# Kernel tuning notes

Hardware: AMD Instinct MI355X
Metric: run time of the kernel (lower is better)

## Reference

```python
import jax, jax.numpy as jnp
import numpy as np
from jax import lax

H_PARAM = 10
DMAX = 3
L = 2 * H_PARAM * H_PARAM + 2 * H_PARAM + 1  # 221 chain length
HEIGHT = H_PARAM + 1   # 11
WIDTH = 2 * H_PARAM + 1  # 21
B, N = 256, 128
INIT_STD = 1e-9


def setup_inputs() -> dict:
    key = jax.random.key(0)
    k1, k2 = jax.random.split(key)
    samples = jax.random.normal(k1, (B, N, HEIGHT, WIDTH, DMAX), dtype=jnp.float32)
    tensors1 = INIT_STD * jax.random.normal(k2, (L, DMAX, DMAX, DMAX), dtype=jnp.float32)
    bias_mat = jnp.eye(DMAX, dtype=jnp.float32)[None, :, :]  # [1, D, D]
    return {"samples": samples, "tensors1": tensors1, "bias_mat": bias_mat}


def reference(samples, tensors1, bias_mat):
    b, n = samples.shape[0], samples.shape[1]
    D = tensors1.shape[-1]
    # [B*N, HW, D] then keep only the L positions actually contracted
    s = samples.reshape(b * n, -1, D)[:, : tensors1.shape[0], :]
    s_seq = jnp.moveaxis(s, 1, 0)  # [L, BN, D]
    eye_bias = bias_mat[0]         # [D, D]
    init = jnp.zeros((b * n, D), dtype=samples.dtype).at[:, 0].set(1.0)

    def step(vec, xs):
        x, T = xs  # x: [BN, D], T: [D, D, D]
        mats = jnp.einsum('bd,lrd->blr', x, T) + eye_bias  # [BN, D, D]
        vec = jnp.einsum('bl,blr->br', vec, mats)          # [BN, D]
        return vec, None

    vec, _ = lax.scan(step, init, (s_seq, tensors1))
    return vec.reshape(b, n, D)
```

## Files before the change

kernel.cpp:

```cpp
#include <hip/hip_runtime.h>

#define BN        32768
#define ESTRIDE   693
#define L_REAL    221
#define CHUNK     14
#define PH        7
#define PDW       21
#define SLICE_DW  1344
#define NGRP      4

__device__ __forceinline__ void dma12(const float* g, float* l) {
    __builtin_amdgcn_global_load_lds(
        (const __attribute__((address_space(1))) void*)g,
        (__attribute__((address_space(3))) void*)l,
        12, 0, 0);
}

__global__ __launch_bounds__(256, 8)
void mps_worker(const float* __restrict__ samples,
                const float* __restrict__ tensors,
                float* __restrict__ ws)
{
    __shared__ float lds_x[4 * SLICE_DW];

    const int tid = threadIdx.x;
    const int eg  = blockIdx.x >> 2;
    const int cg  = blockIdx.x & 3;
    const int e0  = eg * 64;
    const int w   = tid >> 6;
    const int b   = tid & 63;
    const int ck  = __builtin_amdgcn_readfirstlane(cg * 4 + w);

    unsigned g7[7];
    #pragma unroll
    for (int k = 0; k < 7; ++k) {
        int i  = k * 64 + b;
        int e  = i / 7;
        int pc = i - e * 7;
        g7[k] = (unsigned)(e0 + e) * ESTRIDE + (unsigned)(ck * (CHUNK * 3) + pc * 3);
    }

    float* slice = lds_x + w * SLICE_DW;
    float P[9] = {1.f, 0.f, 0.f, 0.f, 1.f, 0.f, 0.f, 0.f, 1.f};

    #pragma unroll
    for (int k = 0; k < 7; ++k)
        dma12(samples + g7[k], slice + k * 192);

    #pragma unroll
    for (int p = 0; p < 2; ++p) {
        asm volatile("s_waitcnt vmcnt(0)" ::: "memory");
        __builtin_amdgcn_sched_barrier(0);

        float xq[PDW];
        const float* Xs = slice + b * PDW;
        #pragma unroll
        for (int j = 0; j < PDW; ++j) xq[j] = Xs[j];
        asm volatile("s_waitcnt lgkmcnt(0)" ::: "memory");
        __builtin_amdgcn_sched_barrier(0);

        if (p == 0) {
            #pragma unroll
            for (int k = 0; k < 7; ++k)
                dma12(samples + g7[k] + PDW, slice + k * 192);
        }

        #pragma unroll
        for (int s = 0; s < PH; ++s) {
            const int l = ck * CHUNK + p * PH + s;
            if (l < L_REAL) {
                const float* Tg = tensors + l * 27;
                float Ts[27];
                #pragma unroll
                for (int j = 0; j < 27; ++j) Ts[j] = Tg[j];

                const float x0 = xq[s * 3 + 0];
                const float x1 = xq[s * 3 + 1];
                const float x2 = xq[s * 3 + 2];

                float E[9];
                #pragma unroll
                for (int l2 = 0; l2 < 3; ++l2)
                    #pragma unroll
                    for (int r = 0; r < 3; ++r)
                        E[l2 * 3 + r] = x0 * Ts[l2 * 9 + r * 3 + 0]
                                      + x1 * Ts[l2 * 9 + r * 3 + 1]
                                      + x2 * Ts[l2 * 9 + r * 3 + 2];

                float PN[9];
                #pragma unroll
                for (int i = 0; i < 3; ++i)
                    #pragma unroll
                    for (int r = 0; r < 3; ++r)
                        PN[i * 3 + r] = P[i * 3 + 0] * E[0 + r]
                                      + P[i * 3 + 1] * E[3 + r]
                                      + P[i * 3 + 2] * E[6 + r];
                #pragma unroll
                for (int k = 0; k < 9; ++k) P[k] += PN[k];
            }
        }
    }

    __syncthreads();
    {
        float* pb = lds_x + tid * 9;
        #pragma unroll
        for (int k = 0; k < 9; ++k) pb[k] = P[k];
    }
    __syncthreads();

    if (tid < 64) {
        float G[9];
        #pragma unroll
        for (int k = 0; k < 9; ++k) G[k] = lds_x[tid * 9 + k];
        #pragma unroll
        for (int w2 = 1; w2 < 4; ++w2) {
            const float* q = lds_x + (w2 * 64 + tid) * 9;
            float N[9];
            #pragma unroll
            for (int i = 0; i < 3; ++i)
                #pragma unroll
                for (int r = 0; r < 3; ++r)
                    N[i * 3 + r] = G[i * 3 + 0] * q[0 + r]
                                 + G[i * 3 + 1] * q[3 + r]
                                 + G[i * 3 + 2] * q[6 + r];
            #pragma unroll
            for (int k = 0; k < 9; ++k) G[k] = N[k];
        }
        #pragma unroll
        for (int k = 0; k < 9; ++k)
            ws[((size_t)(cg * 9 + k) << 15) + (size_t)(e0 + tid)] = G[k];
    }
}

__global__ __launch_bounds__(256)
void mps_combine(const float* __restrict__ ws, float* __restrict__ out)
{
    const int e = blockIdx.x * 256 + threadIdx.x;
    float v0 = ws[(size_t)(0 << 15) + e];
    float v1 = ws[(size_t)(1 << 15) + e];
    float v2 = ws[(size_t)(2 << 15) + e];
    #pragma unroll
    for (int g = 1; g < NGRP; ++g) {
        float q[9];
        #pragma unroll
        for (int k = 0; k < 9; ++k)
            q[k] = ws[((size_t)(g * 9 + k) << 15) + e];
        float n0 = v0 * q[0] + v1 * q[3] + v2 * q[6];
        float n1 = v0 * q[1] + v1 * q[4] + v2 * q[7];
        float n2 = v0 * q[2] + v1 * q[5] + v2 * q[8];
        v0 = n0; v1 = n1; v2 = n2;
    }
    float* o = out + (size_t)e * 3;
    o[0] = v0; o[1] = v1; o[2] = v2;
}

extern "C" void kernel_launch(void* const* d_in, const int* in_sizes, int n_in,
                              void* d_out, int out_size, void* d_ws, size_t ws_size,
                              hipStream_t stream)
{
    const float* samples = (const float*)d_in[0];
    const float* tensors = (const float*)d_in[1];
    float* out = (float*)d_out;
    float* ws  = (float*)d_ws;
    (void)ws_size;

    mps_worker<<<dim3(512 * NGRP), dim3(256), 0, stream>>>(samples, tensors, ws);
    mps_combine<<<dim3(BN / 256), dim3(256), 0, stream>>>(ws, out);
}
```

Baseline: 35.21 us.

## Replace LDS DMA staging with direct per-thread global loads of sample chunk

Drops the two-phase global_load_lds staging of sample slices through LDS and instead has each thread load its 42 contiguous floats straight from global memory into registers, then run all 14 chain steps in one loop. This removes the LDS round trip, explicit waitcnt barriers and the mid-kernel double-buffer reissue. It shrinks LDS use and lowers the occupancy hint from 8 to 6 waves to allow more registers. The cost is that per-thread loads with a 693-float stride are poorly coalesced, and register pressure rises.

```diff
diff --git a/kernel.cpp b/kernel.cpp
--- a/kernel.cpp
+++ b/kernel.cpp
@@ -4,24 +4,15 @@
 #define ESTRIDE   693
 #define L_REAL    221
 #define CHUNK     14
-#define PH        7
-#define PDW       21
-#define SLICE_DW  1344
+#define CDW       42
 #define NGRP      4
 
-__device__ __forceinline__ void dma12(const float* g, float* l) {
-    __builtin_amdgcn_global_load_lds(
-        (const __attribute__((address_space(1))) void*)g,
-        (__attribute__((address_space(3))) void*)l,
-        12, 0, 0);
-}
-
-__global__ __launch_bounds__(256, 8)
+__global__ __launch_bounds__(256, 6)
 void mps_worker(const float* __restrict__ samples,
                 const float* __restrict__ tensors,
                 float* __restrict__ ws)
 {
-    __shared__ float lds_x[4 * SLICE_DW];
+    __shared__ float lds_p[256 * 9];
 
     const int tid = threadIdx.x;
     const int eg  = blockIdx.x >> 2;
@@ -31,79 +22,47 @@
     const int b   = tid & 63;
     const int ck  = __builtin_amdgcn_readfirstlane(cg * 4 + w);
 
-    unsigned g7[7];
+    const float* xp = samples + (size_t)(e0 + b) * ESTRIDE + ck * CDW;
+    float xq[CDW];
     #pragma unroll
-    for (int k = 0; k < 7; ++k) {
-        int i  = k * 64 + b;
-        int e  = i / 7;
-        int pc = i - e * 7;
-        g7[k] = (unsigned)(e0 + e) * ESTRIDE + (unsigned)(ck * (CHUNK * 3) + pc * 3);
-    }
+    for (int j = 0; j < CDW; ++j) xq[j] = xp[j];
 
-    float* slice = lds_x + w * SLICE_DW;
     float P[9] = {1.f, 0.f, 0.f, 0.f, 1.f, 0.f, 0.f, 0.f, 1.f};
 
     #pragma unroll
-    for (int k = 0; k < 7; ++k)
-        dma12(samples + g7[k], slice + k * 192);
+    for (int s = 0; s < CHUNK; ++s) {
+        const int l = ck * CHUNK + s;
+        if (l < L_REAL) {
+            const float* Tg = tensors + l * 27;
+            float Ts[27];
+            #pragma unroll
+            for (int j = 0; j < 27; ++j) Ts[j] = Tg[j];
 
-    #pragma unroll
-    for (int p = 0; p < 2; ++p) {
-        asm volatile("s_waitcnt vmcnt(0)" ::: "memory");
-        __builtin_amdgcn_sched_barrier(0);
+            const float x0 = xq[s * 3 + 0];
+            const float x1 = xq[s * 3 + 1];
+            const float x2 = xq[s * 3 + 2];
 
-        float xq[PDW];
-        const float* Xs = slice + b * PDW;
-        #pragma unroll
-        for (int j = 0; j < PDW; ++j) xq[j] = Xs[j];
-        asm volatile("s_waitcnt lgkmcnt(0)" ::: "memory");
-        __builtin_amdgcn_sched_barrier(0);
+            float E[9];
+            #pragma unroll
+            for (int l2 = 0; l2 < 3; ++l2)
+                #pragma unroll
+                for (int r = 0; r < 3; ++r)
+                    E[l2 * 3 + r] = x0 * Ts[l2 * 9 + r * 3 + 0]
+                                  + x1 * Ts[l2 * 9 + r * 3 + 1]
+                                  + x2 * Ts[l2 * 9 + r * 3 + 2];
 
-        if (p == 0) {
             #pragma unroll
-            for (int k = 0; k < 7; ++k)
-                dma12(samples + g7[k] + PDW, slice + k * 192);
-        }
-
-        #pragma unroll
-        for (int s = 0; s < PH; ++s) {
-            const int l = ck * CHUNK + p * PH + s;
-            if (l < L_REAL) {
-                const float* Tg = tensors + l * 27;
-                float Ts[27];
-                #pragma unroll
-                for (int j = 0; j < 27; ++j) Ts[j] = Tg[j];
-
-                const float x0 = xq[s * 3 + 0];
-                const float x1 = xq[s * 3 + 1];
-                const float x2 = xq[s * 3 + 2];
-
-                float E[9];
-                #pragma unroll
-                for (int l2 = 0; l2 < 3; ++l2)
-                    #pragma unroll
-                    for (int r = 0; r < 3; ++r)
-                        E[l2 * 3 + r] = x0 * Ts[l2 * 9 + r * 3 + 0]
-                                      + x1 * Ts[l2 * 9 + r * 3 + 1]
-                                      + x2 * Ts[l2 * 9 + r * 3 + 2];
-
-                float PN[9];
-                #pragma unroll
-                for (int i = 0; i < 3; ++i)
-                    #pragma unroll
-                    for (int r = 0; r < 3; ++r)
-                        PN[i * 3 + r] = P[i * 3 + 0] * E[0 + r]
-                                      + P[i * 3 + 1] * E[3 + r]
-                                      + P[i * 3 + 2] * E[6 + r];
-                #pragma unroll
-                for (int k = 0; k < 9; ++k) P[k] += PN[k];
+            for (int i = 0; i < 3; ++i) {
+                const float p0 = P[i * 3 + 0], p1 = P[i * 3 + 1], p2 = P[i * 3 + 2];
+                P[i * 3 + 0] = p0 + (p0 * E[0] + p1 * E[3] + p2 * E[6]);
+                P[i * 3 + 1] = p1 + (p0 * E[1] + p1 * E[4] + p2 * E[7]);
+                P[i * 3 + 2] = p2 + (p0 * E[2] + p1 * E[5] + p2 * E[8]);
             }
         }
     }
 
-    __syncthreads();
     {
-        float* pb = lds_x + tid * 9;
+        float* pb = lds_p + tid * 9;
         #pragma unroll
         for (int k = 0; k < 9; ++k) pb[k] = P[k];
     }
@@ -112,10 +71,10 @@
     if (tid < 64) {
         float G[9];
         #pragma unroll
-        for (int k = 0; k < 9; ++k) G[k] = lds_x[tid * 9 + k];
+        for (int k = 0; k < 9; ++k) G[k] = lds_p[tid * 9 + k];
         #pragma unroll
         for (int w2 = 1; w2 < 4; ++w2) {
-            const float* q = lds_x + (w2 * 64 + tid) * 9;
+            const float* q = lds_p + (w2 * 64 + tid) * 9;
             float N[9];
             #pragma unroll
             for (int i = 0; i < 3; ++i)
```

Measured after the change: 30.50 us. 13.4% less time.
